# Performance work log

Hardware: AMD Instinct MI355X
Metric: run time of the kernel (lower is better)

Reference implementation:

```python
import jax, jax.numpy as jnp
import numpy as np

B = 8192
NOISE = 25


def setup_inputs() -> dict:
    key = jax.random.key(0)
    ks = jax.random.split(key, 16)
    rn = lambda k, s: jax.random.normal(k, s, dtype=jnp.float32)
    return {
        "z": rn(ks[0], (B, 3)),
        "z_next": rn(ks[1], (B, 3)),
        "n": rn(ks[2], (B, NOISE)),
        "prior": rn(ks[3], (B, 4611)),
        "w1_W": rn(ks[4], (NOISE, 192)) * 0.2, "w1_b": rn(ks[5], (192,)) * 0.1,
        "b1_W": rn(ks[6], (NOISE, 64)) * 0.2, "b1_b": rn(ks[7], (64,)) * 0.1,
        "w2_W": rn(ks[8], (NOISE, 4096)) * 0.2, "w2_b": rn(ks[9], (4096,)) * 0.1,
        "b2_W": rn(ks[10], (NOISE, 64)) * 0.2, "b2_b": rn(ks[11], (64,)) * 0.1,
        "w3_W": rn(ks[12], (NOISE, 192)) * 0.2, "w3_b": rn(ks[13], (192,)) * 0.1,
        "b3_W": rn(ks[14], (NOISE, 3)) * 0.2, "b3_b": rn(ks[15], (3,)) * 0.1,
    }


def _pairwise_dist(A, Bm):
    # sqrt(sum_d (A_i - B_j)^2 + 1e-8) computed via the norm identity -> one GEMM
    sq = (jnp.sum(A * A, axis=1)[:, None]
          + jnp.sum(Bm * Bm, axis=1)[None, :]
          - 2.0 * (A @ Bm.T))
    return jnp.sqrt(jnp.maximum(sq, 0.0) + 1e-8)


def reference(z, z_next, n, prior,
              w1_W, w1_b, b1_W, b1_b,
              w2_W, w2_b, b2_W, b2_b,
              w3_W, w3_b, b3_W, b3_b):
    bs = z.shape[0]
    # hypernetwork: per-sample decoder weights from noise n (B, 25)
    W1 = (n @ w1_W + w1_b).reshape(bs, 64, 3)
    B1 = n @ b1_W + b1_b                       # (B, 64)
    W2 = (n @ w2_W + w2_b).reshape(bs, 64, 64)
    B2 = n @ b2_W + b2_b                       # (B, 64)
    W3 = (n @ w3_W + w3_b).reshape(bs, 3, 64)
    B3 = n @ b3_W + b3_b                       # (B, 3)
    # decode: per-sample bmm chain with ELU
    h = jax.nn.elu(jnp.einsum('bij,bj->bi', W1, z) + B1)
    h = jax.nn.elu(jnp.einsum('bij,bj->bi', W2, h) + B2)
    z_hat = jnp.einsum('bij,bj->bi', W3, h) + B3
    recon = jnp.mean(jnp.sum((z_hat - z_next) ** 2, axis=1))
    # KL estimator over flattened generated weights, D = 4611
    G = jnp.concatenate([W1.reshape(bs, -1), B1, W2.reshape(bs, -1), B2,
                         W3.reshape(bs, -1), B3], axis=1)
    wp = jnp.min(_pairwise_dist(prior, G), axis=0)   # nearest prior sample per gen sample
    idx = jnp.arange(bs)
    ww_mat = _pairwise_dist(G, G).at[idx, idx].add(1e10)
    ww = jnp.min(ww_mat, axis=0)
    D = G.shape[1]
    kl = jnp.mean(jnp.log(wp / (ww + 1e-8) + 1e-8)) * D
    kl = kl + jnp.log(jnp.float32(bs) / jnp.float32(bs - 1))
    return recon, kl, z_hat
```

## Files before the change

kernel.cpp:

```cpp
#include <hip/hip_runtime.h>
#include <math.h>

#define BATCH 8192
#define D_G   4611
#define DGP   4624
#define KN    25
#define KE    28

#define WS_WCAT   0
#define WS_BCAT   115600
#define WS_WCATT  120224
#define WS_M      249344
#define WS_C      249984
#define WS_BB     250016
#define WS_PPAD   250048
#define WS_Q      479424
#define WS_G2     487616
#define WS_RPAD   495808
#define WS_WP2    725184
#define WS_WW2    733376
#define WS_ACC    741568
#define WS_H1T    741600
#define WS_H2T    1265888

__device__ inline float eluf(float x) { return x > 0.f ? x : expm1f(x); }

__device__ __forceinline__ void gload_lds16(const float* g, float* l) {
  __builtin_amdgcn_global_load_lds((const __attribute__((address_space(1))) unsigned int*)g,
                                   (__attribute__((address_space(3))) unsigned int*)l, 16, 0, 0);
}

__device__ inline float sdot26(const float* __restrict__ WT, int rowidx, const float* nx) {
  const float* row = WT + (size_t)__builtin_amdgcn_readfirstlane(rowidx) * KE;
  float acc = row[25];
#pragma unroll
  for (int k = 0; k < 25; k++) acc = fmaf(row[k], nx[k], acc);
  return acc;
}

__global__ void k_init(float* ws) {
  int idx = blockIdx.x * 256 + threadIdx.x;
  unsigned int* u = (unsigned int*)ws;
  if (idx < BATCH)            u[WS_WP2 + idx] = 0x7F7FFFFFu;
  else if (idx < 2 * BATCH)   u[WS_WW2 + (idx - BATCH)] = 0x7F7FFFFFu;
  else if (idx == 2 * BATCH)  ws[WS_ACC] = 0.f;
}

__global__ void k_build(const float* __restrict__ w1W, const float* __restrict__ w1b,
                        const float* __restrict__ b1W, const float* __restrict__ b1b,
                        const float* __restrict__ w2W, const float* __restrict__ w2b,
                        const float* __restrict__ b2W, const float* __restrict__ b2b,
                        const float* __restrict__ w3W, const float* __restrict__ w3b,
                        const float* __restrict__ b3W, const float* __restrict__ b3b,
                        float* ws) {
  int idx = blockIdx.x * 256 + threadIdx.x;
  if (idx >= KN * D_G) return;
  int k = idx / D_G;
  int d = idx - k * D_G;
  float wv, bv;
  if (d < 192)       { int c = d;        wv = w1W[k*192  + c]; bv = w1b[c]; }
  else if (d < 256)  { int c = d - 192;  wv = b1W[k*64   + c]; bv = b1b[c]; }
  else if (d < 4352) { int c = d - 256;  wv = w2W[k*4096 + c]; bv = w2b[c]; }
  else if (d < 4416) { int c = d - 4352; wv = b2W[k*64   + c]; bv = b2b[c]; }
  else if (d < 4608) { int c = d - 4416; wv = w3W[k*192  + c]; bv = w3b[c]; }
  else               { int c = d - 4608; wv = b3W[k*3    + c]; bv = b3b[c]; }
  ws[WS_WCAT  + k * DGP + d] = wv;
  ws[WS_WCATT + d * KE  + k] = wv;
  if (k == 0) {
    ws[WS_BCAT + d] = bv;
    ws[WS_WCATT + d * KE + 25] = bv;
    ws[WS_WCATT + d * KE + 26] = 0.f;
    ws[WS_WCATT + d * KE + 27] = 0.f;
  }
}

__global__ __launch_bounds__(256) void k_M(float* ws) {
  const float* Wc = ws + WS_WCAT;
  const float* bc = ws + WS_BCAT;
  __shared__ float part[4][26];
  int a = blockIdx.x, t = threadIdx.x;
  int wv = t >> 6, l = t & 63;
  if (a < 25) {
    float acc[26];
#pragma unroll
    for (int v = 0; v < 26; v++) acc[v] = 0.f;
    for (int d = t; d < D_G; d += 256) {
      float va = Wc[a * DGP + d];
#pragma unroll
      for (int b = 0; b < 25; b++) acc[b] += va * Wc[b * DGP + d];
      acc[25] += va * bc[d];
    }
#pragma unroll
    for (int v = 0; v < 26; v++) {
      float x = acc[v];
#pragma unroll
      for (int off = 32; off > 0; off >>= 1) x += __shfl_down(x, off, 64);
      if (l == 0) part[wv][v] = x;
    }
    __syncthreads();
    if (t < 26) {
      float s = part[0][t] + part[1][t] + part[2][t] + part[3][t];
      if (t < 25) ws[WS_M + a * 25 + t] = s; else ws[WS_C + a] = s;
    }
  } else {
    float acc = 0.f;
    for (int d = t; d < D_G; d += 256) { float b = bc[d]; acc += b * b; }
#pragma unroll
    for (int off = 32; off > 0; off >>= 1) acc += __shfl_down(acc, off, 64);
    if (l == 0) part[wv][0] = acc;
    __syncthreads();
    if (t == 0) ws[WS_BB] = part[0][0] + part[1][0] + part[2][0] + part[3][0];
  }
}

__global__ void k_persample(const float* __restrict__ n, float* ws) {
  int j = blockIdx.x * 256 + threadIdx.x;
  if (j >= BATCH) return;
  const float* M  = ws + WS_M;
  const float* cv = ws + WS_C;
  float nr[25];
#pragma unroll
  for (int k = 0; k < 25; k++) nr[k] = n[j * 25 + k];
  float q = 0.f;
  for (int k2 = 0; k2 < 25; k2++) {
    float p = 0.f;
#pragma unroll
    for (int k1 = 0; k1 < 25; k1++) p += nr[k1] * M[k1 * 25 + k2];
    ws[WS_PPAD + j * KE + k2] = p;
    q += p * nr[k2];
  }
  float nc = 0.f;
#pragma unroll
  for (int k = 0; k < 25; k++) nc += nr[k] * cv[k];
  ws[WS_PPAD + j * KE + 25] = -0.5f * q;
  ws[WS_PPAD + j * KE + 26] = 0.f;
  ws[WS_PPAD + j * KE + 27] = 0.f;
  ws[WS_Q  + j] = q;
  ws[WS_G2 + j] = q + 2.f * nc + ws[WS_BB];
}

__global__ __launch_bounds__(256, 2) void k_prior(const float* __restrict__ prior, float* ws) {
  __shared__ float wlds[2][26 * 256 + 512];
  const float* wc = ws + WS_WCAT;
  const float* bc = ws + WS_BCAT;
  int t = threadIdx.x;
  int wv = t >> 6, l = t & 63;
  int i0 = (blockIdx.x * 4 + wv) * 4;
  const float* pr0 = prior + (size_t)i0 * D_G;

  float racc[4][25];
  float sacc[4], p2acc[4];
#pragma unroll
  for (int r = 0; r < 4; r++) {
    sacc[r] = 0.f; p2acc[r] = 0.f;
#pragma unroll
    for (int k = 0; k < 25; k++) racc[r][k] = 0.f;
  }

  float pvC[4][4], pvN[4][4];

#pragma unroll
  for (int u = 0; u < 7; u++) {
    int row = u * 4 + wv;
    if (row < 26)
      gload_lds16(wc + (size_t)row * DGP + 4 * l, &wlds[0][row * 256]);
  }
#pragma unroll
  for (int r = 0; r < 4; r++)
#pragma unroll
    for (int q = 0; q < 4; q++)
      pvN[r][q] = pr0[(size_t)r * D_G + 4 * l + q];

  for (int ch = 0; ch < 18; ++ch) {
    int cur = ch & 1;
    __syncthreads();
#pragma unroll
    for (int r = 0; r < 4; r++)
#pragma unroll
      for (int q = 0; q < 4; q++) pvC[r][q] = pvN[r][q];
    if (ch < 17) {
      int dnext = (ch + 1) * 256;
#pragma unroll
      for (int u = 0; u < 7; u++) {
        int row = u * 4 + wv;
        if (row < 26)
          gload_lds16(wc + (size_t)row * DGP + dnext + 4 * l, &wlds[cur ^ 1][row * 256]);
      }
#pragma unroll
      for (int r = 0; r < 4; r++)
#pragma unroll
        for (int q = 0; q < 4; q++)
          pvN[r][q] = pr0[(size_t)r * D_G + dnext + 4 * l + q];
    }
    const float* wb = wlds[cur];
    float4 bl = *(const float4*)&wb[25 * 256 + 4 * l];
#pragma unroll
    for (int r = 0; r < 4; r++) {
      p2acc[r] += pvC[r][0]*pvC[r][0] + pvC[r][1]*pvC[r][1] + pvC[r][2]*pvC[r][2] + pvC[r][3]*pvC[r][3];
      sacc[r]  += pvC[r][0]*bl.x + pvC[r][1]*bl.y + pvC[r][2]*bl.z + pvC[r][3]*bl.w;
    }
#pragma unroll
    for (int k = 0; k < 25; k++) {
      float4 w = *(const float4*)&wb[k * 256 + 4 * l];
#pragma unroll
      for (int r = 0; r < 4; r++)
        racc[r][k] += pvC[r][0]*w.x + pvC[r][1]*w.y + pvC[r][2]*w.z + pvC[r][3]*w.w;
    }
  }
  if (l < 3) {
    int d = 4608 + l;
#pragma unroll
    for (int r = 0; r < 4; r++) {
      float pvt = pr0[(size_t)r * D_G + d];
      p2acc[r] += pvt * pvt;
      sacc[r]  += pvt * bc[d];
#pragma unroll
      for (int k = 0; k < 25; k++) racc[r][k] += pvt * wc[(size_t)k * DGP + d];
    }
  }
#pragma unroll
  for (int r = 0; r < 4; r++) {
#pragma unroll
    for (int k = 0; k < 25; k++) {
      float v = racc[r][k];
#pragma unroll
      for (int off = 32; off > 0; off >>= 1) v += __shfl_down(v, off, 64);
      if (l == 0) ws[WS_RPAD + (size_t)(i0 + r) * KE + k] = v;
    }
    float s = sacc[r], p2 = p2acc[r];
#pragma unroll
    for (int off = 32; off > 0; off >>= 1) { s += __shfl_down(s, off, 64); p2 += __shfl_down(p2, off, 64); }
    if (l == 0) {
      ws[WS_RPAD + (size_t)(i0 + r) * KE + 25] = -0.5f * (p2 - 2.f * s);
      ws[WS_RPAD + (size_t)(i0 + r) * KE + 26] = 0.f;
      ws[WS_RPAD + (size_t)(i0 + r) * KE + 27] = 0.f;
    }
  }
}

template <int SKIP>
__global__ __launch_bounds__(256) void k_pair(const float* __restrict__ APAD,
                                              const float* __restrict__ Bn,
                                              const float* __restrict__ beta,
                                              unsigned int* __restrict__ outm) {
  __shared__ float rows[256 * KE];
  int t = threadIdx.x;
  int jbase = blockIdx.y * 256;
  {
    const float4* src = (const float4*)(APAD + (size_t)jbase * KE);
    float4* dst = (float4*)rows;
#pragma unroll
    for (int u = 0; u < 7; u++) dst[t + 256 * u] = src[t + 256 * u];
  }
  int j0 = blockIdx.x * 512 + t;
  int j1 = j0 + 256;
  float nx0[25], nx1[25];
#pragma unroll
  for (int k = 0; k < 25; k++) { nx0[k] = Bn[j0 * 25 + k]; nx1[k] = Bn[j1 * 25 + k]; }
  float bj0 = beta[j0], bj1 = beta[j1];
  float mn0 = 3.402823466e38f, mn1 = 3.402823466e38f;
  __syncthreads();
#pragma unroll 2
  for (int it = 0; it < 256; ++it) {
    const float* row = rows + it * KE;
    float a0 = row[25], a1 = row[25];
#pragma unroll
    for (int k = 0; k < 25; k++) { a0 = fmaf(row[k], nx0[k], a0); a1 = fmaf(row[k], nx1[k], a1); }
    float sq0 = fmaxf(fmaf(-2.f, a0, bj0), 0.f);
    float sq1 = fmaxf(fmaf(-2.f, a1, bj1), 0.f);
    int i = jbase + it;
    bool sk0 = SKIP && (i == j0);
    bool sk1 = SKIP && (i == j1);
    mn0 = sk0 ? mn0 : fminf(mn0, sq0);
    mn1 = sk1 ? mn1 : fminf(mn1, sq1);
  }
  atomicMin(&outm[j0], __float_as_uint(mn0));
  atomicMin(&outm[j1], __float_as_uint(mn1));
}

__global__ __launch_bounds__(64) void kd1(const float* __restrict__ n, const float* __restrict__ z,
                                          const float* __restrict__ ws_wt, float* __restrict__ h1t) {
  int s = blockIdx.x * 64 + threadIdx.x;
  int rb = blockIdx.y * 16;
  float nx[25];
#pragma unroll
  for (int k = 0; k < 25; k++) nx[k] = n[s * 25 + k];
  float zr[3];
#pragma unroll
  for (int d = 0; d < 3; d++) zr[d] = z[s * 3 + d];
  for (int r = 0; r < 16; r++) {
    int rr = rb + r;
    float acc = sdot26(ws_wt, 192 + rr, nx);
#pragma unroll
    for (int d = 0; d < 3; d++)
      acc = fmaf(sdot26(ws_wt, rr * 3 + d, nx), zr[d], acc);
    h1t[rr * BATCH + s] = eluf(acc);
  }
}

__global__ __launch_bounds__(64) void kd2(const float* __restrict__ n,
                                          const float* __restrict__ ws_wt,
                                          const float* __restrict__ h1t, float* __restrict__ h2t) {
  int s = blockIdx.x * 64 + threadIdx.x;
  int rb = blockIdx.y * 4;
  float nx[25];
#pragma unroll
  for (int k = 0; k < 25; k++) nx[k] = n[s * 25 + k];
  float acc[4];
#pragma unroll
  for (int r = 0; r < 4; r++) acc[r] = sdot26(ws_wt, 4352 + rb + r, nx);
  for (int c = 0; c < 64; c++) {
    float h1c = h1t[c * BATCH + s];
#pragma unroll
    for (int r = 0; r < 4; r++) {
      float w = sdot26(ws_wt, 256 + (rb + r) * 64 + c, nx);
      acc[r] = fmaf(w, h1c, acc[r]);
    }
  }
#pragma unroll
  for (int r = 0; r < 4; r++) h2t[(rb + r) * BATCH + s] = eluf(acc[r]);
}

__global__ __launch_bounds__(64) void kd3(const float* __restrict__ n,
                                          const float* __restrict__ znext,
                                          const float* __restrict__ ws_wt,
                                          const float* __restrict__ h2t,
                                          float* __restrict__ out, float* __restrict__ accum) {
  int s = blockIdx.x * 64 + threadIdx.x;
  int r = blockIdx.y;
  float nx[25];
#pragma unroll
  for (int k = 0; k < 25; k++) nx[k] = n[s * 25 + k];
  float acc = sdot26(ws_wt, 4608 + r, nx);
  for (int c = 0; c < 64; c++)
    acc = fmaf(sdot26(ws_wt, 4416 + r * 64 + c, nx), h2t[c * BATCH + s], acc);
  out[2 + s * 3 + r] = acc;
  float dz = acc - znext[s * 3 + r];
  float v = dz * dz;
#pragma unroll
  for (int off = 32; off > 0; off >>= 1) v += __shfl_down(v, off, 64);
  if (threadIdx.x == 0) atomicAdd(accum, v);
}

__global__ void k_finish(float* ws, float* __restrict__ out) {
  __shared__ float sred[256];
  int t = threadIdx.x;
  float part = 0.f;
  for (int j = t; j < BATCH; j += 256) {
    float wp2 = ws[WS_WP2 + j];
    float ww2 = ws[WS_WW2 + j];
    float wp = sqrtf(wp2 + 1e-8f);
    float ww = sqrtf(ww2 + 1e-8f);
    part += logf(wp / (ww + 1e-8f) + 1e-8f);
  }
  sred[t] = part; __syncthreads();
  for (int off = 128; off > 0; off >>= 1) { if (t < off) sred[t] += sred[t + off]; __syncthreads(); }
  if (t == 0) {
    float kl = sred[0] / (float)BATCH * (float)D_G + logf((float)BATCH / (float)(BATCH - 1));
    out[0] = ws[WS_ACC] / (float)BATCH;
    out[1] = kl;
  }
}

extern "C" void kernel_launch(void* const* d_in, const int* in_sizes, int n_in,
                              void* d_out, int out_size, void* d_ws, size_t ws_size,
                              hipStream_t stream) {
  (void)in_sizes; (void)n_in; (void)out_size; (void)ws_size;
  const float* z     = (const float*)d_in[0];
  const float* znext = (const float*)d_in[1];
  const float* n     = (const float*)d_in[2];
  const float* prior = (const float*)d_in[3];
  const float* w1W = (const float*)d_in[4];  const float* w1b = (const float*)d_in[5];
  const float* b1W = (const float*)d_in[6];  const float* b1b = (const float*)d_in[7];
  const float* w2W = (const float*)d_in[8];  const float* w2b = (const float*)d_in[9];
  const float* b2W = (const float*)d_in[10]; const float* b2b = (const float*)d_in[11];
  const float* w3W = (const float*)d_in[12]; const float* w3b = (const float*)d_in[13];
  const float* b3W = (const float*)d_in[14]; const float* b3b = (const float*)d_in[15];
  float* out = (float*)d_out;
  float* ws  = (float*)d_ws;

  k_init<<<dim3(65), dim3(256), 0, stream>>>(ws);
  k_build<<<dim3((KN * D_G + 255) / 256), dim3(256), 0, stream>>>(
      w1W, w1b, b1W, b1b, w2W, w2b, b2W, b2b, w3W, w3b, b3W, b3b, ws);
  k_M<<<dim3(26), dim3(256), 0, stream>>>(ws);
  k_persample<<<dim3(32), dim3(256), 0, stream>>>(n, ws);
  k_prior<<<dim3(512), dim3(256), 0, stream>>>(prior, ws);
  k_pair<1><<<dim3(16, 32), dim3(256), 0, stream>>>(ws + WS_PPAD, n, ws + WS_Q,
                                                    (unsigned int*)(ws + WS_WW2));
  k_pair<0><<<dim3(16, 32), dim3(256), 0, stream>>>(ws + WS_RPAD, n, ws + WS_G2,
                                                    (unsigned int*)(ws + WS_WP2));
  kd1<<<dim3(128, 4), dim3(64), 0, stream>>>(n, z, ws + WS_WCATT, ws + WS_H1T);
  kd2<<<dim3(128, 16), dim3(64), 0, stream>>>(n, ws + WS_WCATT, ws + WS_H1T, ws + WS_H2T);
  kd3<<<dim3(128, 3), dim3(64), 0, stream>>>(n, znext, ws + WS_WCATT, ws + WS_H2T, out, ws + WS_ACC);
  k_finish<<<dim3(1), dim3(256), 0, stream>>>(ws, out);
}
```

Before: 545.2 us.

## Stage prior-kernel weight tiles through registers instead of direct global-to-LDS loads

Replaces the global_load_lds double-buffered staging of the weight tile in k_prior with a register-staged pipeline. Each iteration loads the next chunk into registers, computes on the current LDS buffer, then writes the registers into the other buffer, using manual lgkmcnt waits and raw s_barrier. The loop is unrolled by two so the prior row fragments ping-pong between two named register sets instead of being copied. This adds register pressure (7 float4s plus a second prior set) under launch_bounds(256,2), and the barrier sequence relies on the compiler having drained the global loads before the LDS writes.

```diff
diff --git a/kernel.cpp b/kernel.cpp
--- a/kernel.cpp
+++ b/kernel.cpp
@@ -24,11 +24,6 @@
 #define WS_H2T    1265888
 
 __device__ inline float eluf(float x) { return x > 0.f ? x : expm1f(x); }
-
-__device__ __forceinline__ void gload_lds16(const float* g, float* l) {
-  __builtin_amdgcn_global_load_lds((const __attribute__((address_space(1))) unsigned int*)g,
-                                   (__attribute__((address_space(3))) unsigned int*)l, 16, 0, 0);
-}
 
 __device__ inline float sdot26(const float* __restrict__ WT, int rowidx, const float* nx) {
   const float* row = WT + (size_t)__builtin_amdgcn_readfirstlane(rowidx) * KE;
@@ -140,7 +135,7 @@
 }
 
 __global__ __launch_bounds__(256, 2) void k_prior(const float* __restrict__ prior, float* ws) {
-  __shared__ float wlds[2][26 * 256 + 512];
+  __shared__ float wlds[2][26 * 256 + 16];
   const float* wc = ws + WS_WCAT;
   const float* bc = ws + WS_BCAT;
   int t = threadIdx.x;
@@ -157,56 +152,72 @@
     for (int k = 0; k < 25; k++) racc[r][k] = 0.f;
   }
 
-  float pvC[4][4], pvN[4][4];
-
-#pragma unroll
-  for (int u = 0; u < 7; u++) {
-    int row = u * 4 + wv;
-    if (row < 26)
-      gload_lds16(wc + (size_t)row * DGP + 4 * l, &wlds[0][row * 256]);
-  }
-#pragma unroll
-  for (int r = 0; r < 4; r++)
-#pragma unroll
-    for (int q = 0; q < 4; q++)
-      pvN[r][q] = pr0[(size_t)r * D_G + 4 * l + q];
-
-  for (int ch = 0; ch < 18; ++ch) {
-    int cur = ch & 1;
-    __syncthreads();
+  float pvA[4][4], pvB[4][4];
+  float4 wreg[7];
+
+  auto stage_regs = [&](int ch) {
+#pragma unroll
+    for (int u = 0; u < 7; u++) {
+      int row = u * 4 + wv;
+      if (row < 26)
+        wreg[u] = *(const float4*)(wc + (size_t)row * DGP + ch * 256 + 4 * l);
+    }
+  };
+  auto dswrite = [&](float* buf) {
+#pragma unroll
+    for (int u = 0; u < 7; u++) {
+      int row = u * 4 + wv;
+      if (row < 26)
+        *(float4*)&buf[row * 256 + 4 * l] = wreg[u];
+    }
+  };
+  auto loadpv = [&](float (&pv)[4][4], int ch) {
 #pragma unroll
     for (int r = 0; r < 4; r++)
 #pragma unroll
-      for (int q = 0; q < 4; q++) pvC[r][q] = pvN[r][q];
-    if (ch < 17) {
-      int dnext = (ch + 1) * 256;
-#pragma unroll
-      for (int u = 0; u < 7; u++) {
-        int row = u * 4 + wv;
-        if (row < 26)
-          gload_lds16(wc + (size_t)row * DGP + dnext + 4 * l, &wlds[cur ^ 1][row * 256]);
-      }
-#pragma unroll
-      for (int r = 0; r < 4; r++)
-#pragma unroll
-        for (int q = 0; q < 4; q++)
-          pvN[r][q] = pr0[(size_t)r * D_G + dnext + 4 * l + q];
-    }
-    const float* wb = wlds[cur];
+      for (int q = 0; q < 4; q++)
+        pv[r][q] = pr0[(size_t)r * D_G + ch * 256 + 4 * l + q];
+  };
+  auto compute = [&](const float* wb, float (&pv)[4][4]) {
     float4 bl = *(const float4*)&wb[25 * 256 + 4 * l];
 #pragma unroll
     for (int r = 0; r < 4; r++) {
-      p2acc[r] += pvC[r][0]*pvC[r][0] + pvC[r][1]*pvC[r][1] + pvC[r][2]*pvC[r][2] + pvC[r][3]*pvC[r][3];
-      sacc[r]  += pvC[r][0]*bl.x + pvC[r][1]*bl.y + pvC[r][2]*bl.z + pvC[r][3]*bl.w;
+      p2acc[r] += pv[r][0]*pv[r][0] + pv[r][1]*pv[r][1] + pv[r][2]*pv[r][2] + pv[r][3]*pv[r][3];
+      sacc[r]  += pv[r][0]*bl.x + pv[r][1]*bl.y + pv[r][2]*bl.z + pv[r][3]*bl.w;
     }
 #pragma unroll
     for (int k = 0; k < 25; k++) {
       float4 w = *(const float4*)&wb[k * 256 + 4 * l];
 #pragma unroll
       for (int r = 0; r < 4; r++)
-        racc[r][k] += pvC[r][0]*w.x + pvC[r][1]*w.y + pvC[r][2]*w.z + pvC[r][3]*w.w;
-    }
-  }
+        racc[r][k] += pv[r][0]*w.x + pv[r][1]*w.y + pv[r][2]*w.z + pv[r][3]*w.w;
+    }
+  };
+
+  stage_regs(0);
+  loadpv(pvA, 0);
+  dswrite(wlds[0]);
+  asm volatile("s_waitcnt lgkmcnt(0)" ::: "memory");
+  __builtin_amdgcn_s_barrier();
+  asm volatile("" ::: "memory");
+
+  for (int it = 0; it < 9; ++it) {
+    int c1 = 2 * it + 1;
+    stage_regs(c1);
+    loadpv(pvB, c1);
+    compute(wlds[0], pvA);
+    dswrite(wlds[1]);
+    asm volatile("s_waitcnt lgkmcnt(0)" ::: "memory");
+    __builtin_amdgcn_s_barrier();
+    asm volatile("" ::: "memory");
+    if (c1 < 17) { stage_regs(c1 + 1); loadpv(pvA, c1 + 1); }
+    compute(wlds[1], pvB);
+    if (c1 < 17) dswrite(wlds[0]);
+    asm volatile("s_waitcnt lgkmcnt(0)" ::: "memory");
+    __builtin_amdgcn_s_barrier();
+    asm volatile("" ::: "memory");
+  }
+
   if (l < 3) {
     int d = 4608 + l;
 #pragma unroll
```

After: 895.4 us. 1.64x slower.

## Merge pair kernels into one launch, fold init into build, use scalar loads

Applied to the files above, without the earlier changes.

Folds the workspace initialisation into the build kernel and merges the two pairwise-min kernels into a single launch that uses the z grid dimension to pick the operands. The pair kernel no longer stages rows in shared memory; it reads each row through wave-uniform (readfirstlane) loads via sdot26, which removes the LDS copy and the block barrier. This cuts two launches and doubles the blocks available in one grid. The risk is that the scalar-memory path is slower than LDS reads in the inner loop.

```diff
diff --git a/kernel.cpp b/kernel.cpp
--- a/kernel.cpp
+++ b/kernel.cpp
@@ -38,14 +38,6 @@
   return acc;
 }
 
-__global__ void k_init(float* ws) {
-  int idx = blockIdx.x * 256 + threadIdx.x;
-  unsigned int* u = (unsigned int*)ws;
-  if (idx < BATCH)            u[WS_WP2 + idx] = 0x7F7FFFFFu;
-  else if (idx < 2 * BATCH)   u[WS_WW2 + (idx - BATCH)] = 0x7F7FFFFFu;
-  else if (idx == 2 * BATCH)  ws[WS_ACC] = 0.f;
-}
-
 __global__ void k_build(const float* __restrict__ w1W, const float* __restrict__ w1b,
                         const float* __restrict__ b1W, const float* __restrict__ b1b,
                         const float* __restrict__ w2W, const float* __restrict__ w2b,
@@ -54,6 +46,10 @@
                         const float* __restrict__ b3W, const float* __restrict__ b3b,
                         float* ws) {
   int idx = blockIdx.x * 256 + threadIdx.x;
+  unsigned int* u = (unsigned int*)ws;
+  if (idx < BATCH)            u[WS_WP2 + idx] = 0x7F7FFFFFu;
+  else if (idx < 2 * BATCH)   u[WS_WW2 + (idx - BATCH)] = 0x7F7FFFFFu;
+  else if (idx == 2 * BATCH)  ws[WS_ACC] = 0.f;
   if (idx >= KN * D_G) return;
   int k = idx / D_G;
   int d = idx - k * D_G;
@@ -238,20 +234,20 @@
   }
 }
 
-template <int SKIP>
-__global__ __launch_bounds__(256) void k_pair(const float* __restrict__ APAD,
-                                              const float* __restrict__ Bn,
-                                              const float* __restrict__ beta,
-                                              unsigned int* __restrict__ outm) {
-  __shared__ float rows[256 * KE];
+__global__ __launch_bounds__(256) void k_pair2(const float* __restrict__ ppad,
+                                               const float* __restrict__ rpad,
+                                               const float* __restrict__ Bn,
+                                               const float* __restrict__ qv,
+                                               const float* __restrict__ g2v,
+                                               unsigned int* __restrict__ ww2,
+                                               unsigned int* __restrict__ wp2) {
+  int zsel = blockIdx.z;
+  const float* APAD = zsel ? rpad : ppad;
+  const float* beta = zsel ? g2v  : qv;
+  unsigned int* outm = zsel ? wp2 : ww2;
+  bool doskip = (zsel == 0);
   int t = threadIdx.x;
   int jbase = blockIdx.y * 256;
-  {
-    const float4* src = (const float4*)(APAD + (size_t)jbase * KE);
-    float4* dst = (float4*)rows;
-#pragma unroll
-    for (int u = 0; u < 7; u++) dst[t + 256 * u] = src[t + 256 * u];
-  }
   int j0 = blockIdx.x * 512 + t;
   int j1 = j0 + 256;
   float nx0[25], nx1[25];
@@ -259,18 +255,15 @@
   for (int k = 0; k < 25; k++) { nx0[k] = Bn[j0 * 25 + k]; nx1[k] = Bn[j1 * 25 + k]; }
   float bj0 = beta[j0], bj1 = beta[j1];
   float mn0 = 3.402823466e38f, mn1 = 3.402823466e38f;
-  __syncthreads();
 #pragma unroll 2
   for (int it = 0; it < 256; ++it) {
-    const float* row = rows + it * KE;
-    float a0 = row[25], a1 = row[25];
-#pragma unroll
-    for (int k = 0; k < 25; k++) { a0 = fmaf(row[k], nx0[k], a0); a1 = fmaf(row[k], nx1[k], a1); }
+    int i = jbase + it;
+    float a0 = sdot26(APAD, i, nx0);
+    float a1 = sdot26(APAD, i, nx1);
     float sq0 = fmaxf(fmaf(-2.f, a0, bj0), 0.f);
     float sq1 = fmaxf(fmaf(-2.f, a1, bj1), 0.f);
-    int i = jbase + it;
-    bool sk0 = SKIP && (i == j0);
-    bool sk1 = SKIP && (i == j1);
+    bool sk0 = doskip && (i == j0);
+    bool sk1 = doskip && (i == j1);
     mn0 = sk0 ? mn0 : fminf(mn0, sq0);
     mn1 = sk1 ? mn1 : fminf(mn1, sq1);
   }
@@ -379,16 +372,14 @@
   float* out = (float*)d_out;
   float* ws  = (float*)d_ws;
 
-  k_init<<<dim3(65), dim3(256), 0, stream>>>(ws);
   k_build<<<dim3((KN * D_G + 255) / 256), dim3(256), 0, stream>>>(
       w1W, w1b, b1W, b1b, w2W, w2b, b2W, b2b, w3W, w3b, b3W, b3b, ws);
   k_M<<<dim3(26), dim3(256), 0, stream>>>(ws);
   k_persample<<<dim3(32), dim3(256), 0, stream>>>(n, ws);
   k_prior<<<dim3(512), dim3(256), 0, stream>>>(prior, ws);
-  k_pair<1><<<dim3(16, 32), dim3(256), 0, stream>>>(ws + WS_PPAD, n, ws + WS_Q,
-                                                    (unsigned int*)(ws + WS_WW2));
-  k_pair<0><<<dim3(16, 32), dim3(256), 0, stream>>>(ws + WS_RPAD, n, ws + WS_G2,
-                                                    (unsigned int*)(ws + WS_WP2));
+  k_pair2<<<dim3(16, 32, 2), dim3(256), 0, stream>>>(
+      ws + WS_PPAD, ws + WS_RPAD, n, ws + WS_Q, ws + WS_G2,
+      (unsigned int*)(ws + WS_WW2), (unsigned int*)(ws + WS_WP2));
   kd1<<<dim3(128, 4), dim3(64), 0, stream>>>(n, z, ws + WS_WCATT, ws + WS_H1T);
   kd2<<<dim3(128, 16), dim3(64), 0, stream>>>(n, ws + WS_WCATT, ws + WS_H1T, ws + WS_H2T);
   kd3<<<dim3(128, 3), dim3(64), 0, stream>>>(n, znext, ws + WS_WCATT, ws + WS_H2T, out, ws + WS_ACC);
```

After: 585.7 us. 7.4% more time.
